# Performance work log

Hardware: AMD Instinct MI355X
Metric: run time of the kernel (lower is better)

Reference implementation:

```python
import jax, jax.numpy as jnp
import numpy as np

N_NODES = 50000
N_EDGES = 800000
D = 128
N_REL = 4
N_GRAPHS = 128
N_CLASSES = 16


def rgcn_layer(x, W_rel, W_root, b, src, dst, edge_type):
    # Per-relation transform of all nodes: [N, R, D]
    xt = jnp.einsum('nd,rdf->nrf', x, W_rel)
    msg = xt[src, edge_type]  # [E, D] gather message per edge
    # mean aggregation per (dst, relation) pair (PyG RGCNConv aggr='mean')
    seg = dst * N_REL + edge_type
    cnt = jax.ops.segment_sum(jnp.ones((src.shape[0],), x.dtype), seg,
                              num_segments=N_NODES * N_REL)
    norm = 1.0 / jnp.maximum(cnt[seg], 1.0)
    agg = jax.ops.segment_sum(msg * norm[:, None], dst, num_segments=N_NODES)
    return agg + x @ W_root + b


def setup_inputs() -> dict:
    key = jax.random.key(0)
    ks = jax.random.split(key, 12)
    s = 1.0 / np.sqrt(D)
    inp = {
        'x': jax.random.normal(ks[0], (N_NODES, D), jnp.float32),
        'edge_index': jax.random.randint(ks[1], (2, N_EDGES), 0, N_NODES, jnp.int64),
        'edge_type': jax.random.randint(ks[2], (N_EDGES,), 0, N_REL, jnp.int64),
        'batch': jnp.sort(jax.random.randint(ks[3], (N_NODES,), 0, N_GRAPHS, jnp.int64)),
        'W_rel1': jax.random.normal(ks[4], (N_REL, D, D), jnp.float32) * s,
        'W_root1': jax.random.normal(ks[5], (D, D), jnp.float32) * s,
        'b1': jnp.zeros((D,), jnp.float32),
        'W_rel2': jax.random.normal(ks[6], (N_REL, D, D), jnp.float32) * s,
        'W_root2': jax.random.normal(ks[7], (D, D), jnp.float32) * s,
        'b2': jnp.zeros((D,), jnp.float32),
        'W_cls': jax.random.normal(ks[8], (D, N_CLASSES), jnp.float32) * s,
        'b_cls': jnp.zeros((N_CLASSES,), jnp.float32),
    }
    return inp


def reference(x, edge_index, edge_type, batch, W_rel1, W_root1, b1,
              W_rel2, W_root2, b2, W_cls, b_cls):
    src, dst = edge_index[0], edge_index[1]
    h = jax.nn.relu(rgcn_layer(x, W_rel1, W_root1, b1, src, dst, edge_type))
    h = jax.nn.relu(rgcn_layer(h, W_rel2, W_root2, b2, src, dst, edge_type))
    # global mean pool over graphs (dropout is identity: training=False)
    gsum = jax.ops.segment_sum(h, batch, num_segments=N_GRAPHS)
    gcnt = jax.ops.segment_sum(jnp.ones((h.shape[0],), h.dtype), batch,
                               num_segments=N_GRAPHS)
    g = gsum / jnp.maximum(gcnt, 1.0)[:, None]
    return g @ W_cls + b_cls
```

## Files before the change

### kernel.cpp

```cpp
#include <hip/hip_runtime.h>

#define D_DIM 128
#define N_REL 4
#define CAP 32

typedef __attribute__((ext_vector_type(8))) short bf16x8;
typedef __attribute__((ext_vector_type(4))) float f32x4;

static inline int cdiv(int a, int b) { return (a + b - 1) / b; }

__device__ inline ushort f2bf(float f) {
    union { float f; unsigned u; } v;
    v.f = f;
    unsigned r = v.u + 0x7FFFu + ((v.u >> 16) & 1u);
    return (ushort)(r >> 16);
}

__device__ inline float bf2f(ushort u) {
    union { unsigned u; float f; } v;
    v.u = (unsigned)u << 16;
    return v.f;
}

__device__ inline float uif(unsigned u) {
    union { unsigned u; float f; } v;
    v.u = u;
    return v.f;
}

#define CNT_B 391
#define CAST_B 6250
#define PACK_B 80

__global__ __launch_bounds__(256) void prep_kernel(
    const float* __restrict__ x, ushort* __restrict__ Xb,
    const int* __restrict__ src, const int* __restrict__ dst,
    const int* __restrict__ et, unsigned* __restrict__ icnt,
    int* __restrict__ esorted,
    const float* __restrict__ Wrel1, const float* __restrict__ Wroot1,
    const float* __restrict__ Wrel2, const float* __restrict__ Wroot2,
    ushort* __restrict__ Wpk1, ushort* __restrict__ Wpk2,
    int n4, int nEdges) {
    int b = blockIdx.x;
    if (b < CNT_B) {
        int e = (b * 256 + threadIdx.x) * 8;
        if (e >= nEdges) return;
        if (e + 8 <= nEdges) {
            int4 sA = *(const int4*)(src + e);
            int4 sB = *(const int4*)(src + e + 4);
            int4 dA = *(const int4*)(dst + e);
            int4 dB = *(const int4*)(dst + e + 4);
            int4 tA = *(const int4*)(et + e);
            int4 tB = *(const int4*)(et + e + 4);
            unsigned o0 = atomicAdd(&icnt[dA.x], 1u << (8 * tA.x));
            unsigned o1 = atomicAdd(&icnt[dA.y], 1u << (8 * tA.y));
            unsigned o2 = atomicAdd(&icnt[dA.z], 1u << (8 * tA.z));
            unsigned o3 = atomicAdd(&icnt[dA.w], 1u << (8 * tA.w));
            unsigned o4 = atomicAdd(&icnt[dB.x], 1u << (8 * tB.x));
            unsigned o5 = atomicAdd(&icnt[dB.y], 1u << (8 * tB.y));
            unsigned o6 = atomicAdd(&icnt[dB.z], 1u << (8 * tB.z));
            unsigned o7 = atomicAdd(&icnt[dB.w], 1u << (8 * tB.w));
            int r0 = (int)(((o0 >> (8 * tA.x)) & 0xFFu) - 0xAAu);
            int r1 = (int)(((o1 >> (8 * tA.y)) & 0xFFu) - 0xAAu);
            int r2 = (int)(((o2 >> (8 * tA.z)) & 0xFFu) - 0xAAu);
            int r3 = (int)(((o3 >> (8 * tA.w)) & 0xFFu) - 0xAAu);
            int r4 = (int)(((o4 >> (8 * tB.x)) & 0xFFu) - 0xAAu);
            int r5 = (int)(((o5 >> (8 * tB.y)) & 0xFFu) - 0xAAu);
            int r6 = (int)(((o6 >> (8 * tB.z)) & 0xFFu) - 0xAAu);
            int r7 = (int)(((o7 >> (8 * tB.w)) & 0xFFu) - 0xAAu);
            esorted[((size_t)(dA.x * N_REL + tA.x) << 5) + r0] = sA.x;
            esorted[((size_t)(dA.y * N_REL + tA.y) << 5) + r1] = sA.y;
            esorted[((size_t)(dA.z * N_REL + tA.z) << 5) + r2] = sA.z;
            esorted[((size_t)(dA.w * N_REL + tA.w) << 5) + r3] = sA.w;
            esorted[((size_t)(dB.x * N_REL + tB.x) << 5) + r4] = sB.x;
            esorted[((size_t)(dB.y * N_REL + tB.y) << 5) + r5] = sB.y;
            esorted[((size_t)(dB.z * N_REL + tB.z) << 5) + r6] = sB.z;
            esorted[((size_t)(dB.w * N_REL + tB.w) << 5) + r7] = sB.w;
        } else {
            for (int j = 0; e + j < nEdges; ++j) {
                int dd = dst[e + j], tt = et[e + j];
                unsigned o = atomicAdd(&icnt[dd], 1u << (8 * tt));
                int r = (int)(((o >> (8 * tt)) & 0xFFu) - 0xAAu);
                esorted[((size_t)(dd * N_REL + tt) << 5) + r] = src[e + j];
            }
        }
    } else if (b < CNT_B + CAST_B) {
        int i = (b - CNT_B) * 256 + threadIdx.x;
        if (i < n4) {
            float4 v = ((const float4*)x)[i];
            ushort4 o;
            o.x = f2bf(v.x); o.y = f2bf(v.y); o.z = f2bf(v.z); o.w = f2bf(v.w);
            ((ushort4*)Xb)[i] = o;
        }
    } else {
        int pb = b - (CNT_B + CAST_B);
        int layer = pb / 40;
        int rem = pb % 40;
        int mat = rem >> 3;
        int blk = rem & 7;
        const float* Wrel = layer ? Wrel2 : Wrel1;
        const float* Wroot = layer ? Wroot2 : Wroot1;
        ushort* out = layer ? Wpk2 : Wpk1;
        const float* W = (mat < N_REL) ? (Wrel + (size_t)mat * D_DIM * D_DIM) : Wroot;
        int t = blk * 256 + threadIdx.x;
        int lane = t & 63;
        int tile = t >> 6;
        int kt = tile >> 3;
        int nt = tile & 7;
        int n = nt * 16 + (lane & 15);
        int kb = kt * 32 + (lane >> 4) * 8;
        ushort* o = out + (((size_t)mat * 32 + tile) * 64 + lane) * 8;
        ushort4 lo, hi;
        lo.x = f2bf(W[(kb + 0) * D_DIM + n]);
        lo.y = f2bf(W[(kb + 1) * D_DIM + n]);
        lo.z = f2bf(W[(kb + 2) * D_DIM + n]);
        lo.w = f2bf(W[(kb + 3) * D_DIM + n]);
        hi.x = f2bf(W[(kb + 4) * D_DIM + n]);
        hi.y = f2bf(W[(kb + 5) * D_DIM + n]);
        hi.z = f2bf(W[(kb + 6) * D_DIM + n]);
        hi.w = f2bf(W[(kb + 7) * D_DIM + n]);
        *(ushort4*)(o) = lo;
        *(ushort4*)(o + 4) = hi;
    }
}

__global__ __launch_bounds__(256) void gather_kernel(
    const ushort* __restrict__ Xb, const unsigned* __restrict__ icnt,
    const int* __restrict__ esorted, ushort* __restrict__ M, int nseg) {
    __shared__ int ids[16][CAP];
    __shared__ int sdeg[16];
    __shared__ int perm[16];
    const int tid = threadIdx.x;
    const int ql = tid & 15;
    const int qd = tid >> 4;
    const int seg0 = blockIdx.x * 16;

    if (tid < 16) {
        int seg = seg0 + tid;
        int deg = -1;
        if (seg < nseg) {
            unsigned w = icnt[seg >> 2];
            deg = (int)(((w >> ((seg & 3) * 8)) & 0xFFu) - 0xAAu);
        }
        sdeg[tid] = deg;
    }
    __syncthreads();
    if (tid < 16) {
        int myd = sdeg[tid];
        int rank = 0;
#pragma unroll
        for (int j = 0; j < 16; ++j) {
            int dj = sdeg[j];
            rank += (dj < myd || (dj == myd && j < tid)) ? 1 : 0;
        }
        perm[rank] = tid;
    }
    __syncthreads();

    const int local = perm[qd];
    const int seg = seg0 + local;
    const int deg = sdeg[local];
    if (deg < 0) return;
    uint4* mout = (uint4*)(M + (size_t)seg * D_DIM + ql * 8);
    const ushort* xb = Xb + ql * 8;
    const int* eb = esorted + ((size_t)seg << 5);
    if (deg == 0) {
        *mout = make_uint4(0u, 0u, 0u, 0u);
        return;
    }
    if (deg == 1) {
        *mout = *(const uint4*)(xb + (size_t)eb[0] * D_DIM);
        return;
    }
    for (int j = ql; j < deg; j += 16) ids[qd][j] = eb[j];
    __threadfence_block();
    if (ql == 0) {
        for (int i = 1; i < deg; ++i) {
            int v = ids[qd][i];
            int j = i - 1;
            while (j >= 0 && ids[qd][j] > v) {
                ids[qd][j + 1] = ids[qd][j];
                --j;
            }
            ids[qd][j + 1] = v;
        }
    }
    __threadfence_block();
    float a[8], b[8];
#pragma unroll
    for (int j = 0; j < 8; ++j) { a[j] = 0.f; b[j] = 0.f; }
    auto acc8 = [](float* acc, uint4 u) {
        acc[0] += uif(u.x << 16); acc[1] += uif(u.x & 0xFFFF0000u);
        acc[2] += uif(u.y << 16); acc[3] += uif(u.y & 0xFFFF0000u);
        acc[4] += uif(u.z << 16); acc[5] += uif(u.z & 0xFFFF0000u);
        acc[6] += uif(u.w << 16); acc[7] += uif(u.w & 0xFFFF0000u);
    };
    int e = 0;
    for (; e + 4 <= deg; e += 4) {
        int s0 = ids[qd][e];
        int s1 = ids[qd][e + 1];
        int s2 = ids[qd][e + 2];
        int s3 = ids[qd][e + 3];
        uint4 u0 = *(const uint4*)(xb + (size_t)s0 * D_DIM);
        uint4 u1 = *(const uint4*)(xb + (size_t)s1 * D_DIM);
        uint4 u2 = *(const uint4*)(xb + (size_t)s2 * D_DIM);
        uint4 u3 = *(const uint4*)(xb + (size_t)s3 * D_DIM);
        acc8(a, u0); acc8(b, u1); acc8(a, u2); acc8(b, u3);
    }
    if (e + 2 <= deg) {
        int s0 = ids[qd][e];
        int s1 = ids[qd][e + 1];
        uint4 u0 = *(const uint4*)(xb + (size_t)s0 * D_DIM);
        uint4 u1 = *(const uint4*)(xb + (size_t)s1 * D_DIM);
        acc8(a, u0); acc8(b, u1);
        e += 2;
    }
    if (e < deg) {
        uint4 u0 = *(const uint4*)(xb + (size_t)ids[qd][e] * D_DIM);
        acc8(a, u0);
    }
    float sc = 1.0f / (float)deg;
    uint4 o;
    o.x = (unsigned)f2bf((a[0] + b[0]) * sc) | ((unsigned)f2bf((a[1] + b[1]) * sc) << 16);
    o.y = (unsigned)f2bf((a[2] + b[2]) * sc) | ((unsigned)f2bf((a[3] + b[3]) * sc) << 16);
    o.z = (unsigned)f2bf((a[4] + b[4]) * sc) | ((unsigned)f2bf((a[5] + b[5]) * sc) << 16);
    o.w = (unsigned)f2bf((a[6] + b[6]) * sc) | ((unsigned)f2bf((a[7] + b[7]) * sc) << 16);
    *mout = o;
}

__global__ __launch_bounds__(256) void gemm_kernel(
    const ushort* __restrict__ M, const ushort* __restrict__ Xb,
    const ushort* __restrict__ Wpk, const float* __restrict__ bias,
    ushort* __restrict__ outb, int n_nodes) {
    __shared__ uint4 BsV[2048];
    const int tid = threadIdx.x;
    const int wave = tid >> 6;
    const int lane = tid & 63;
    const int m = lane & 15;
    const int q = lane >> 4;
    const int r0 = blockIdx.x * 64 + wave * 16;
    const int n = min(r0 + m, n_nodes - 1);

    const ushort* aM = M + (size_t)n * (N_REL * D_DIM) + q * 8;
    const ushort* aX = Xb + (size_t)n * D_DIM + q * 8;
    const ushort* Bs = (const ushort*)BsV;

    f32x4 acc[8];
#pragma unroll
    for (int nt = 0; nt < 8; ++nt) acc[nt] = (f32x4){0.f, 0.f, 0.f, 0.f};

    for (int phase = 0; phase < 5; ++phase) {
        const uint4* Wp4 = (const uint4*)(Wpk + (size_t)phase * 32 * 64 * 8);
        __syncthreads();
#pragma unroll
        for (int j = 0; j < 8; ++j) BsV[j * 256 + tid] = Wp4[j * 256 + tid];
        __syncthreads();

        const ushort* ab = (phase < N_REL) ? (aM + phase * D_DIM) : aX;
#pragma unroll
        for (int kt = 0; kt < 4; ++kt) {
            bf16x8 a = *(const bf16x8*)(ab + kt * 32);
#pragma unroll
            for (int nt = 0; nt < 8; ++nt) {
                bf16x8 b = *(const bf16x8*)(Bs + ((size_t)(kt * 8 + nt) * 64 + lane) * 8);
                acc[nt] = __builtin_amdgcn_mfma_f32_16x16x32_bf16(a, b, acc[nt], 0, 0, 0);
            }
        }
    }

#pragma unroll
    for (int nt = 0; nt < 8; ++nt) {
        int col = nt * 16 + m;
        float bv = bias[col];
#pragma unroll
        for (int r = 0; r < 4; ++r) {
            int row = r0 + q * 4 + r;
            if (row < n_nodes)
                outb[(size_t)row * D_DIM + col] = f2bf(fmaxf(acc[nt][r] + bv, 0.0f));
        }
    }
}

__global__ __launch_bounds__(1024) void poolcls_kernel(
    const ushort* __restrict__ hb, const int* __restrict__ batch,
    const float* __restrict__ Wcls, const float* __restrict__ bcls,
    float* __restrict__ out, int n_nodes) {
    __shared__ float part[8][D_DIM];
    __shared__ float mean[D_DIM];
    __shared__ float cpart[16][17];
    int g = blockIdx.x;
    int tid = threadIdx.x;
    int d = tid & 127;
    int par = tid >> 7;
    auto lb = [&](int val) {
        int lo = 0, hi = n_nodes;
        while (lo < hi) {
            int mid = (lo + hi) >> 1;
            if (batch[mid] < val) lo = mid + 1; else hi = mid;
        }
        return lo;
    };
    int lo = lb(g), hi = lb(g + 1);
    float aa = 0.f;
    for (int nn = lo + par; nn < hi; nn += 8)
        aa += bf2f(hb[(size_t)nn * D_DIM + d]);
    part[par][d] = aa;
    __syncthreads();
    if (par == 0)
        mean[d] = (((part[0][d] + part[1][d]) + (part[2][d] + part[3][d])) +
                   ((part[4][d] + part[5][d]) + (part[6][d] + part[7][d]))) /
                  fmaxf((float)(hi - lo), 1.0f);
    __syncthreads();
    if (tid < 256) {
        int c = tid & 15, kc = tid >> 4;
        float s = 0.f;
#pragma unroll
        for (int j = 0; j < 8; ++j)
            s = fmaf(mean[kc * 8 + j], Wcls[(kc * 8 + j) * 16 + c], s);
        cpart[kc][c] = s;
    }
    __syncthreads();
    if (tid < 16) {
        float s = bcls[tid];
#pragma unroll
        for (int k = 0; k < 16; ++k) s += cpart[k][tid];
        out[g * 16 + tid] = s;
    }
}

extern "C" void kernel_launch(void* const* d_in, const int* in_sizes, int n_in,
                              void* d_out, int out_size, void* d_ws, size_t ws_size,
                              hipStream_t stream) {
    const float* x      = (const float*)d_in[0];
    const int*   ei     = (const int*)d_in[1];
    const int*   etype  = (const int*)d_in[2];
    const int*   batch  = (const int*)d_in[3];
    const float* Wrel1  = (const float*)d_in[4];
    const float* Wroot1 = (const float*)d_in[5];
    const float* b1     = (const float*)d_in[6];
    const float* Wrel2  = (const float*)d_in[7];
    const float* Wroot2 = (const float*)d_in[8];
    const float* b2     = (const float*)d_in[9];
    const float* Wcls   = (const float*)d_in[10];
    const float* bcls   = (const float*)d_in[11];
    float* out = (float*)d_out;

    const int N = in_sizes[0] / D_DIM;
    const int E = in_sizes[1] / 2;
    const int NSEG = N * N_REL;
    const int* src = ei;
    const int* dst = ei + E;

    ushort* Xb   = (ushort*)d_ws;
    ushort* h1b  = Xb + (size_t)N * D_DIM;
    ushort* h2b  = h1b + (size_t)N * D_DIM;
    ushort* M    = h2b + (size_t)N * D_DIM;
    ushort* Wpk1 = M + (size_t)N * N_REL * D_DIM;
    ushort* Wpk2 = Wpk1 + 81920;
    unsigned* icnt = (unsigned*)(Wpk2 + 81920);
    int* esorted = (int*)(icnt + N);

    prep_kernel<<<CNT_B + CAST_B + PACK_B, 256, 0, stream>>>(
        x, Xb, src, dst, etype, icnt, esorted, Wrel1, Wroot1, Wrel2, Wroot2,
        Wpk1, Wpk2, N * D_DIM / 4, E);

    gather_kernel<<<cdiv(NSEG, 16), 256, 0, stream>>>(
        Xb, icnt, esorted, M, NSEG);
    gemm_kernel<<<cdiv(N, 64), 256, 0, stream>>>(M, Xb, Wpk1, b1, h1b, N);

    gather_kernel<<<cdiv(NSEG, 16), 256, 0, stream>>>(
        h1b, icnt, esorted, M, NSEG);
    gemm_kernel<<<cdiv(N, 64), 256, 0, stream>>>(M, h1b, Wpk2, b2, h2b, N);

    poolcls_kernel<<<128, 1024, 0, stream>>>(h2b, batch, Wcls, bcls, out, N);
}
```

Baseline: 296.9 us.

## Parallelize segment sort, drop LDS staging in GEMM, vectorize pooling

The gather kernel replaces the single-lane insertion sort of neighbor ids with a parallel rank sort in which each lane computes its element's rank and scatters it to a second shared array. The GEMM kernel no longer stages the weights in LDS with block barriers. Each wave now computes a 32-row by 64-column tile and reads the packed B fragments straight from global memory, relying on cache. The pooling kernel uses 64 node partitions with 8-wide vectorized bf16 loads and a padded shared reduction. These changes cut serial sort work, barrier stalls and scalar loads, at the cost of more global or L2 traffic for the weights.

```diff
diff --git a/kernel.cpp b/kernel.cpp
--- a/kernel.cpp
+++ b/kernel.cpp
@@ -128,6 +128,7 @@
     const ushort* __restrict__ Xb, const unsigned* __restrict__ icnt,
     const int* __restrict__ esorted, ushort* __restrict__ M, int nseg) {
     __shared__ int ids[16][CAP];
+    __shared__ int sids[16][CAP];
     __shared__ int sdeg[16];
     __shared__ int perm[16];
     const int tid = threadIdx.x;
@@ -174,15 +175,17 @@
     }
     for (int j = ql; j < deg; j += 16) ids[qd][j] = eb[j];
     __threadfence_block();
-    if (ql == 0) {
-        for (int i = 1; i < deg; ++i) {
-            int v = ids[qd][i];
-            int j = i - 1;
-            while (j >= 0 && ids[qd][j] > v) {
-                ids[qd][j + 1] = ids[qd][j];
-                --j;
+#pragma unroll
+    for (int base = 0; base < 2; ++base) {
+        int j = base * 16 + ql;
+        if (j < deg) {
+            int v = ids[qd][j];
+            int rank = 0;
+            for (int k = 0; k < deg; ++k) {
+                int w = ids[qd][k];
+                rank += (w < v || (w == v && k < j)) ? 1 : 0;
             }
-            ids[qd][j + 1] = v;
+            sids[qd][rank] = v;
         }
     }
     __threadfence_block();
@@ -197,10 +200,10 @@
     };
     int e = 0;
     for (; e + 4 <= deg; e += 4) {
-        int s0 = ids[qd][e];
-        int s1 = ids[qd][e + 1];
-        int s2 = ids[qd][e + 2];
-        int s3 = ids[qd][e + 3];
+        int s0 = sids[qd][e];
+        int s1 = sids[qd][e + 1];
+        int s2 = sids[qd][e + 2];
+        int s3 = sids[qd][e + 3];
         uint4 u0 = *(const uint4*)(xb + (size_t)s0 * D_DIM);
         uint4 u1 = *(const uint4*)(xb + (size_t)s1 * D_DIM);
         uint4 u2 = *(const uint4*)(xb + (size_t)s2 * D_DIM);
@@ -208,15 +211,15 @@
         acc8(a, u0); acc8(b, u1); acc8(a, u2); acc8(b, u3);
     }
     if (e + 2 <= deg) {
-        int s0 = ids[qd][e];
-        int s1 = ids[qd][e + 1];
+        int s0 = sids[qd][e];
+        int s1 = sids[qd][e + 1];
         uint4 u0 = *(const uint4*)(xb + (size_t)s0 * D_DIM);
         uint4 u1 = *(const uint4*)(xb + (size_t)s1 * D_DIM);
         acc8(a, u0); acc8(b, u1);
         e += 2;
     }
     if (e < deg) {
-        uint4 u0 = *(const uint4*)(xb + (size_t)ids[qd][e] * D_DIM);
+        uint4 u0 = *(const uint4*)(xb + (size_t)sids[qd][e] * D_DIM);
         acc8(a, u0);
     }
     float sc = 1.0f / (float)deg;
@@ -232,51 +235,58 @@
     const ushort* __restrict__ M, const ushort* __restrict__ Xb,
     const ushort* __restrict__ Wpk, const float* __restrict__ bias,
     ushort* __restrict__ outb, int n_nodes) {
-    __shared__ uint4 BsV[2048];
     const int tid = threadIdx.x;
     const int wave = tid >> 6;
     const int lane = tid & 63;
     const int m = lane & 15;
     const int q = lane >> 4;
-    const int r0 = blockIdx.x * 64 + wave * 16;
-    const int n = min(r0 + m, n_nodes - 1);
-
-    const ushort* aM = M + (size_t)n * (N_REL * D_DIM) + q * 8;
-    const ushort* aX = Xb + (size_t)n * D_DIM + q * 8;
-    const ushort* Bs = (const ushort*)BsV;
-
-    f32x4 acc[8];
-#pragma unroll
-    for (int nt = 0; nt < 8; ++nt) acc[nt] = (f32x4){0.f, 0.f, 0.f, 0.f};
+    const int rh = wave >> 1;
+    const int nh = wave & 1;
+    const int r0 = blockIdx.x * 64 + rh * 32;
+    const int n0 = min(r0 + m, n_nodes - 1);
+    const int n1 = min(r0 + 16 + m, n_nodes - 1);
+
+    const ushort* aM0 = M + (size_t)n0 * (N_REL * D_DIM) + q * 8;
+    const ushort* aM1 = M + (size_t)n1 * (N_REL * D_DIM) + q * 8;
+    const ushort* aX0 = Xb + (size_t)n0 * D_DIM + q * 8;
+    const ushort* aX1 = Xb + (size_t)n1 * D_DIM + q * 8;
+
+    f32x4 acc[2][4];
+#pragma unroll
+    for (int h = 0; h < 2; ++h)
+#pragma unroll
+        for (int j = 0; j < 4; ++j) acc[h][j] = (f32x4){0.f, 0.f, 0.f, 0.f};
 
     for (int phase = 0; phase < 5; ++phase) {
-        const uint4* Wp4 = (const uint4*)(Wpk + (size_t)phase * 32 * 64 * 8);
-        __syncthreads();
-#pragma unroll
-        for (int j = 0; j < 8; ++j) BsV[j * 256 + tid] = Wp4[j * 256 + tid];
-        __syncthreads();
-
-        const ushort* ab = (phase < N_REL) ? (aM + phase * D_DIM) : aX;
+        const ushort* Bp = Wpk + (size_t)phase * 32 * 64 * 8;
+        const ushort* ab0 = (phase < N_REL) ? (aM0 + phase * D_DIM) : aX0;
+        const ushort* ab1 = (phase < N_REL) ? (aM1 + phase * D_DIM) : aX1;
 #pragma unroll
         for (int kt = 0; kt < 4; ++kt) {
-            bf16x8 a = *(const bf16x8*)(ab + kt * 32);
-#pragma unroll
-            for (int nt = 0; nt < 8; ++nt) {
-                bf16x8 b = *(const bf16x8*)(Bs + ((size_t)(kt * 8 + nt) * 64 + lane) * 8);
-                acc[nt] = __builtin_amdgcn_mfma_f32_16x16x32_bf16(a, b, acc[nt], 0, 0, 0);
+            bf16x8 a0 = *(const bf16x8*)(ab0 + kt * 32);
+            bf16x8 a1 = *(const bf16x8*)(ab1 + kt * 32);
+#pragma unroll
+            for (int j = 0; j < 4; ++j) {
+                int nt = nh * 4 + j;
+                bf16x8 b = *(const bf16x8*)(Bp + ((size_t)(kt * 8 + nt) * 64 + lane) * 8);
+                acc[0][j] = __builtin_amdgcn_mfma_f32_16x16x32_bf16(a0, b, acc[0][j], 0, 0, 0);
+                acc[1][j] = __builtin_amdgcn_mfma_f32_16x16x32_bf16(a1, b, acc[1][j], 0, 0, 0);
             }
         }
     }
 
 #pragma unroll
-    for (int nt = 0; nt < 8; ++nt) {
-        int col = nt * 16 + m;
+    for (int j = 0; j < 4; ++j) {
+        int col = (nh * 4 + j) * 16 + m;
         float bv = bias[col];
 #pragma unroll
-        for (int r = 0; r < 4; ++r) {
-            int row = r0 + q * 4 + r;
-            if (row < n_nodes)
-                outb[(size_t)row * D_DIM + col] = f2bf(fmaxf(acc[nt][r] + bv, 0.0f));
+        for (int h = 0; h < 2; ++h) {
+#pragma unroll
+            for (int r = 0; r < 4; ++r) {
+                int row = r0 + h * 16 + q * 4 + r;
+                if (row < n_nodes)
+                    outb[(size_t)row * D_DIM + col] = f2bf(fmaxf(acc[h][j][r] + bv, 0.0f));
+            }
         }
     }
 }
@@ -285,13 +295,13 @@
     const ushort* __restrict__ hb, const int* __restrict__ batch,
     const float* __restrict__ Wcls, const float* __restrict__ bcls,
     float* __restrict__ out, int n_nodes) {
-    __shared__ float part[8][D_DIM];
+    __shared__ float part[64][D_DIM + 1];
     __shared__ float mean[D_DIM];
     __shared__ float cpart[16][17];
     int g = blockIdx.x;
     int tid = threadIdx.x;
-    int d = tid & 127;
-    int par = tid >> 7;
+    int par = tid >> 4;
+    int dg = (tid & 15) * 8;
     auto lb = [&](int val) {
         int lo = 0, hi = n_nodes;
         while (lo < hi) {
@@ -301,15 +311,25 @@
         return lo;
     };
     int lo = lb(g), hi = lb(g + 1);
-    float aa = 0.f;
-    for (int nn = lo + par; nn < hi; nn += 8)
-        aa += bf2f(hb[(size_t)nn * D_DIM + d]);
-    part[par][d] = aa;
-    __syncthreads();
-    if (par == 0)
-        mean[d] = (((part[0][d] + part[1][d]) + (part[2][d] + part[3][d])) +
-                   ((part[4][d] + part[5][d]) + (part[6][d] + part[7][d]))) /
-                  fmaxf((float)(hi - lo), 1.0f);
+    float a[8];
+#pragma unroll
+    for (int j = 0; j < 8; ++j) a[j] = 0.f;
+    for (int nn = lo + par; nn < hi; nn += 64) {
+        uint4 u = *(const uint4*)(hb + (size_t)nn * D_DIM + dg);
+        a[0] += uif(u.x << 16); a[1] += uif(u.x & 0xFFFF0000u);
+        a[2] += uif(u.y << 16); a[3] += uif(u.y & 0xFFFF0000u);
+        a[4] += uif(u.z << 16); a[5] += uif(u.z & 0xFFFF0000u);
+        a[6] += uif(u.w << 16); a[7] += uif(u.w & 0xFFFF0000u);
+    }
+#pragma unroll
+    for (int j = 0; j < 8; ++j) part[par][dg + j] = a[j];
+    __syncthreads();
+    if (tid < D_DIM) {
+        float s = 0.f;
+#pragma unroll
+        for (int j = 0; j < 64; ++j) s += part[j][tid];
+        mean[tid] = s / fmaxf((float)(hi - lo), 1.0f);
+    }
     __syncthreads();
     if (tid < 256) {
         int c = tid & 15, kc = tid >> 4;
```

New measurement: 295.9 us. Within noise of the previous version (-0.4%).
